# Kernel optimization log

Hardware: AMD Instinct MI355X
Metric: run time of the kernel (lower is better)

The kernel has to match this reference:

```python
import jax, jax.numpy as jnp
import numpy as np

DIM = 1024
DIM_HEAD = 64
HEADS = 16
INNER = DIM_HEAD * HEADS  # 1024
B, N1, N2 = 8, 4096, 256
EPS = 1e-5


def layer_norm(x, w, b):
    mu = jnp.mean(x, axis=-1, keepdims=True)
    var = jnp.var(x, axis=-1, keepdims=True)
    return (x - mu) * jax.lax.rsqrt(var + EPS) * w + b


def setup_inputs() -> dict:
    key = jax.random.key(0)
    ks = jax.random.split(key, 10)
    return {
        "x": jax.random.normal(ks[0], (B, N1, DIM), jnp.float32),
        "latents": jax.random.normal(ks[1], (B, N2, DIM), jnp.float32),
        "shift": jax.random.normal(ks[2], (B, DIM), jnp.float32),
        "scale": jax.random.normal(ks[3], (B, DIM), jnp.float32),
        "ln1_w": jnp.ones((DIM,), jnp.float32),
        "ln1_b": jnp.zeros((DIM,), jnp.float32),
        "ln2_w": jnp.ones((DIM,), jnp.float32),
        "ln2_b": jnp.zeros((DIM,), jnp.float32),
        "Wq": jax.random.normal(ks[4], (INNER, DIM), jnp.float32) * 0.02,
        "Wkv": jax.random.normal(ks[5], (2 * INNER, DIM), jnp.float32) * 0.02,
        "Wo": jax.random.normal(ks[6], (DIM, INNER), jnp.float32) * 0.02,
    }


def reference(x, latents, shift, scale, ln1_w, ln1_b, ln2_w, ln2_b, Wq, Wkv, Wo):
    x = layer_norm(x, ln1_w, ln1_b)                      # (b, n1, D)
    lat = layer_norm(latents, ln2_w, ln2_b)              # (b, n2, D)
    lat = lat * (1.0 + scale[:, None, :]) + shift[:, None, :]

    b, n2, _ = lat.shape
    q = jnp.einsum('bld,ed->ble', lat, Wq)               # (b, n2, inner)
    kv_in = jnp.concatenate((x, lat), axis=-2)           # (b, n1+n2, D)
    kv = jnp.einsum('bld,ed->ble', kv_in, Wkv)           # (b, n1+n2, 2*inner)
    k, v = jnp.split(kv, 2, axis=-1)

    def to_heads(t):
        bsz, L, _ = t.shape
        return t.reshape(bsz, L, HEADS, DIM_HEAD).transpose(0, 2, 1, 3)

    q, k, v = to_heads(q), to_heads(k), to_heads(v)      # (b, h, L, dh)
    attn_scale = 1.0 / np.sqrt(np.sqrt(DIM_HEAD)).astype(np.float32)
    logits = jnp.einsum('bhqd,bhkd->bhqk', q * attn_scale, k * attn_scale)
    w = jax.nn.softmax(logits.astype(jnp.float32), axis=-1).astype(logits.dtype)
    out = jnp.einsum('bhqk,bhkd->bhqd', w, v)            # (b, h, n2, dh)
    out = out.transpose(0, 2, 1, 3).reshape(b, n2, INNER)
    return jnp.einsum('ble,de->bld', out, Wo)            # (b, n2, D)
```

## Files before the change

kernel.cpp:

```cpp
#include <hip/hip_runtime.h>
#include <cstdint>
#include <cstddef>

#define B_SZ 8
#define N1 4096
#define N2 256
#define LTOT 4352
#define DIMD 1024
#define HEADS 16
#define DH 64
#define MKV (B_SZ * LTOT)
#define ATILE 64
#define AITERS (LTOT / ATILE)

typedef _Float16 f16;
typedef f16 f16x4_t __attribute__((ext_vector_type(4)));
typedef f16 f16x8_t __attribute__((ext_vector_type(8)));
typedef float f32x4_t __attribute__((ext_vector_type(4)));

__device__ __forceinline__ void g2l16(const void* g, void* l) {
  __builtin_amdgcn_global_load_lds(
      (__attribute__((address_space(1))) void*)g,
      (__attribute__((address_space(3))) void*)l, 16, 0, 0);
}

__global__ __launch_bounds__(256) void ln_mod_kernel(
    const float* __restrict__ x, const float* __restrict__ lat,
    const float* __restrict__ shift, const float* __restrict__ scale,
    const float* __restrict__ ln1w, const float* __restrict__ ln1b,
    const float* __restrict__ ln2w, const float* __restrict__ ln2b,
    f16* __restrict__ kv_in) {
  const int row = blockIdx.x;
  const int b = row / LTOT;
  const int n = row - b * LTOT;
  const int tid = threadIdx.x;
  const bool is_lat = (n >= N1);
  const float* src = is_lat ? (lat + (size_t)(b * N2 + (n - N1)) * DIMD)
                            : (x + (size_t)(b * N1 + n) * DIMD);
  float4 v = ((const float4*)src)[tid];
  float s = v.x + v.y + v.z + v.w;
  float s2 = v.x * v.x + v.y * v.y + v.z * v.z + v.w * v.w;
#pragma unroll
  for (int m = 1; m <= 32; m <<= 1) {
    s += __shfl_xor(s, m, 64);
    s2 += __shfl_xor(s2, m, 64);
  }
  __shared__ float red[8];
  const int wave = tid >> 6;
  if ((tid & 63) == 0) { red[wave * 2] = s; red[wave * 2 + 1] = s2; }
  __syncthreads();
  s = red[0] + red[2] + red[4] + red[6];
  s2 = red[1] + red[3] + red[5] + red[7];
  const float mean = s * (1.0f / DIMD);
  const float var = fmaxf(s2 * (1.0f / DIMD) - mean * mean, 0.0f);
  const float rstd = rsqrtf(var + 1e-5f);
  const float4 w4 = ((const float4*)(is_lat ? ln2w : ln1w))[tid];
  const float4 b4 = ((const float4*)(is_lat ? ln2b : ln1b))[tid];
  float y0 = (v.x - mean) * rstd * w4.x + b4.x;
  float y1 = (v.y - mean) * rstd * w4.y + b4.y;
  float y2 = (v.z - mean) * rstd * w4.z + b4.z;
  float y3 = (v.w - mean) * rstd * w4.w + b4.w;
  if (is_lat) {
    float4 sc = ((const float4*)(scale + (size_t)b * DIMD))[tid];
    float4 sh = ((const float4*)(shift + (size_t)b * DIMD))[tid];
    y0 = y0 * (1.0f + sc.x) + sh.x;
    y1 = y1 * (1.0f + sc.y) + sh.y;
    y2 = y2 * (1.0f + sc.z) + sh.z;
    y3 = y3 * (1.0f + sc.w) + sh.w;
  }
  f16x4_t o = {(f16)y0, (f16)y1, (f16)y2, (f16)y3};
  *(f16x4_t*)(kv_in + (size_t)row * DIMD + tid * 4) = o;
}

__global__ __launch_bounds__(256) void cast_kernel(const float* __restrict__ in,
                                                   f16* __restrict__ out, int n4) {
  const int i = blockIdx.x * 256 + threadIdx.x;
  if (i < n4) {
    float4 v = ((const float4*)in)[i];
    f16x4_t o = {(f16)v.x, (f16)v.y, (f16)v.z, (f16)v.w};
    ((f16x4_t*)out)[i] = o;
  }
}

template <int MODE>
__global__ __launch_bounds__(256) void gemm128(
    const f16* __restrict__ A0, const f16* __restrict__ BT,
    void* __restrict__ out0, void* __restrict__ out1, int nt_base) {
  const int mt = blockIdx.y, nt = nt_base + blockIdx.x;
  const f16* Abase;
  if (MODE == 1) {
    const int bb = mt >> 1;
    Abase = A0 + ((size_t)(bb * LTOT + N1 + (mt & 1) * 128)) * DIMD;
  } else {
    Abase = A0 + (size_t)mt * 128 * DIMD;
  }
  const f16* Bbase = BT + (size_t)nt * 128 * DIMD;
  __shared__ alignas(16) f16 As[128 * 32];
  __shared__ alignas(16) f16 Bs[128 * 32];
  const int tid = threadIdx.x;
  const int wave = tid >> 6, lane = tid & 63;
  const int wm = (wave & 1) * 64, wn = (wave >> 1) * 64;
  const int lrow = lane >> 2, lcol = (lane & 3) * 8;
  const int r16 = lane & 15, g8 = (lane >> 4) * 8, q4 = (lane >> 4) * 4;
  f32x4_t acc[4][4] = {};
  for (int k0 = 0; k0 < DIMD; k0 += 32) {
    __syncthreads();
    g2l16(Abase + (size_t)(wave * 16 + lrow) * DIMD + k0 + lcol, &As[(wave * 16) * 32]);
    g2l16(Abase + (size_t)(64 + wave * 16 + lrow) * DIMD + k0 + lcol, &As[(64 + wave * 16) * 32]);
    g2l16(Bbase + (size_t)(wave * 16 + lrow) * DIMD + k0 + lcol, &Bs[(wave * 16) * 32]);
    g2l16(Bbase + (size_t)(64 + wave * 16 + lrow) * DIMD + k0 + lcol, &Bs[(64 + wave * 16) * 32]);
    __syncthreads();
    f16x8_t a[4], bf[4];
#pragma unroll
    for (int i = 0; i < 4; i++)
      a[i] = *(const f16x8_t*)&As[(wm + i * 16 + r16) * 32 + g8];
#pragma unroll
    for (int j = 0; j < 4; j++)
      bf[j] = *(const f16x8_t*)&Bs[(wn + j * 16 + r16) * 32 + g8];
#pragma unroll
    for (int i = 0; i < 4; i++)
#pragma unroll
      for (int j = 0; j < 4; j++)
        acc[i][j] = __builtin_amdgcn_mfma_f32_16x16x32_f16(a[i], bf[j], acc[i][j], 0, 0, 0);
  }

  if constexpr (MODE == 0) {
    const int m0 = mt * 128;
    const int b = m0 / LTOT;
    const int n0 = m0 - b * LTOT;
    const int e0 = nt * 128;
    if (e0 < 1024) {
      f16* kbuf = (f16*)out0;
#pragma unroll
      for (int i = 0; i < 4; i++) {
        const int n_base = n0 + wm + i * 16 + q4;
#pragma unroll
        for (int j = 0; j < 4; j++) {
          const int e = e0 + wn + j * 16 + r16;
          const int h = e >> 6, d = e & 63;
          const size_t base = ((size_t)(b * HEADS + h) * LTOT);
#pragma unroll
          for (int r = 0; r < 4; r++)
            kbuf[(base + n_base + r) * DH + d] = (f16)acc[i][j][r];
        }
      }
    } else {
      f16* vbuf = (f16*)out1;
      const int e0v = e0 - 1024;
#pragma unroll
      for (int i = 0; i < 4; i++) {
        const int n_base = n0 + wm + i * 16 + q4;
#pragma unroll
        for (int j = 0; j < 4; j++) {
          const int e = e0v + wn + j * 16 + r16;
          const int h = e >> 6, d = e & 63;
          f16x4_t pk = {(f16)acc[i][j][0], (f16)acc[i][j][1],
                        (f16)acc[i][j][2], (f16)acc[i][j][3]};
          *(f16x4_t*)&vbuf[((size_t)(b * HEADS + h) * DH + d) * LTOT + n_base] = pk;
        }
      }
    }
  } else if constexpr (MODE == 1) {
    f16* qbuf = (f16*)out0;
    const int b = mt >> 1;
#pragma unroll
    for (int i = 0; i < 4; i++) {
      const int n_base = (mt & 1) * 128 + wm + i * 16 + q4;
#pragma unroll
      for (int j = 0; j < 4; j++) {
        const int e = nt * 128 + wn + j * 16 + r16;
        const int h = e >> 6, d = e & 63;
#pragma unroll
        for (int r = 0; r < 4; r++)
          qbuf[((size_t)(b * HEADS + h) * N2 + n_base + r) * DH + d] = (f16)acc[i][j][r];
      }
    }
  } else {
    float* outp = (float*)out0;
    const int m0 = mt * 128;
#pragma unroll
    for (int i = 0; i < 4; i++) {
#pragma unroll
      for (int j = 0; j < 4; j++) {
        const int col = nt * 128 + wn + j * 16 + r16;
#pragma unroll
        for (int r = 0; r < 4; r++)
          outp[(size_t)(m0 + wm + i * 16 + q4 + r) * DIMD + col] = acc[i][j][r];
      }
    }
  }
}

__global__ __launch_bounds__(512, 1) void attn_kernel(
    const f16* __restrict__ qbuf, const f16* __restrict__ kbuf,
    const f16* __restrict__ vbuf, f16* __restrict__ attn_out) {
  const int bh = blockIdx.x >> 1;
  const int qt = blockIdx.x & 1;
  const int b = bh >> 4, h = bh & 15;
  const f16* qg = qbuf + ((size_t)bh * N2 + qt * 128) * DH;
  const f16* kg = kbuf + (size_t)bh * LTOT * DH;
  const f16* vg = vbuf + (size_t)bh * DH * LTOT;

  __shared__ alignas(16) f16 Ks[2][4096];
  __shared__ alignas(16) f16 Vs[2][4096];
  __shared__ alignas(16) f16 QP[9216];

  const int tid = threadIdx.x, wave = tid >> 6, lane = tid & 63;
  const int lrow = lane >> 2, lcol = (lane & 3) * 8;
  const int r16 = lane & 15, g8 = (lane >> 4) * 8, q4 = (lane >> 4) * 4;
  f16* Ps = &QP[wave * 1152];

#pragma unroll
  for (int i = 0; i < 2; i++) {
    const int c = wave * 2 + i, s = c >> 3, rb = (c & 7) * 16;
    g2l16(qg + (size_t)(rb + lrow) * DH + s * 32 + lcol, &QP[s * 4096 + rb * 32]);
  }
  auto stage = [&](int kt, int buf) {
    const int s = wave >> 2, rb = (wave & 3) * 16;
    g2l16(kg + (size_t)(kt * ATILE + rb + lrow) * DH + s * 32 + lcol,
          &Ks[buf][s * 2048 + rb * 32]);
    g2l16(vg + (size_t)(rb + lrow) * LTOT + kt * ATILE + s * 32 + lcol,
          &Vs[buf][s * 2048 + rb * 32]);
  };
  stage(0, 0);
  stage(1, 1);
  asm volatile("s_waitcnt vmcnt(4)" ::: "memory");
  asm volatile("s_barrier" ::: "memory");
  f16x8_t bQ[2];
#pragma unroll
  for (int s = 0; s < 2; s++)
    bQ[s] = *(const f16x8_t*)&QP[s * 4096 + (wave * 16 + r16) * 32 + g8];
  asm volatile("s_waitcnt lgkmcnt(0)" ::: "memory");

  f32x4_t oacc[4] = {};
  float mrow = -1e30f, lsum = 0.0f;
  const float SCL = 0.125f * 1.44269504089f;

  for (int kt = 0; kt < AITERS; kt++) {
    const int cur = kt & 1;
    asm volatile("s_waitcnt vmcnt(2)" ::: "memory");
    asm volatile("s_barrier" ::: "memory");
    f32x4_t sacc[4] = {};
#pragma unroll
    for (int s = 0; s < 2; s++) {
      f16x8_t aK[4];
#pragma unroll
      for (int i = 0; i < 4; i++)
        aK[i] = *(const f16x8_t*)&Ks[cur][s * 2048 + (i * 16 + r16) * 32 + g8];
#pragma unroll
      for (int i = 0; i < 4; i++)
        sacc[i] = __builtin_amdgcn_mfma_f32_16x16x32_f16(aK[i], bQ[s], sacc[i], 0, 0, 0);
    }
    float vmax = -1e30f;
#pragma unroll
    for (int i = 0; i < 4; i++)
#pragma unroll
      for (int r = 0; r < 4; r++) vmax = fmaxf(vmax, sacc[i][r]);
    vmax = fmaxf(vmax, __shfl_xor(vmax, 16, 64));
    vmax = fmaxf(vmax, __shfl_xor(vmax, 32, 64));
    const float m_new = fmaxf(mrow, SCL * vmax);
    const float alpha = exp2f(mrow - m_new);
    float psum = 0.0f;
#pragma unroll
    for (int i = 0; i < 4; i++) {
      f16x4_t pk;
#pragma unroll
      for (int r = 0; r < 4; r++) {
        const float p = exp2f(SCL * sacc[i][r] - m_new);
        psum += p;
        pk[r] = (f16)p;
      }
      *(f16x4_t*)&Ps[r16 * 72 + i * 16 + q4] = pk;
    }
    psum += __shfl_xor(psum, 16, 64);
    psum += __shfl_xor(psum, 32, 64);
    lsum = lsum * alpha + psum;
    mrow = m_new;
#pragma unroll
    for (int id = 0; id < 4; id++) oacc[id] *= alpha;
#pragma unroll
    for (int s2 = 0; s2 < 2; s2++) {
      f16x8_t aV[4];
#pragma unroll
      for (int id = 0; id < 4; id++)
        aV[id] = *(const f16x8_t*)&Vs[cur][s2 * 2048 + (id * 16 + r16) * 32 + g8];
      const f16x8_t bP = *(const f16x8_t*)&Ps[r16 * 72 + s2 * 32 + g8];
#pragma unroll
      for (int id = 0; id < 4; id++)
        oacc[id] = __builtin_amdgcn_mfma_f32_16x16x32_f16(aV[id], bP, oacc[id], 0, 0, 0);
    }
    asm volatile("s_waitcnt lgkmcnt(0)" ::: "memory");
    asm volatile("s_barrier" ::: "memory");
    if (kt + 2 < AITERS) stage(kt + 2, cur);
  }
  const float inv = 1.0f / lsum;
  const int q = qt * 128 + wave * 16 + r16;
  const size_t rowbase = ((size_t)(b * N2 + q)) * DIMD + h * DH;
#pragma unroll
  for (int id = 0; id < 4; id++) {
    f16x4_t pk;
#pragma unroll
    for (int r = 0; r < 4; r++) pk[r] = (f16)(oacc[id][r] * inv);
    *(f16x4_t*)&attn_out[rowbase + id * 16 + q4] = pk;
  }
}

extern "C" void kernel_launch(void* const* d_in, const int* in_sizes, int n_in,
                              void* d_out, int out_size, void* d_ws, size_t ws_size,
                              hipStream_t stream) {
  const float* x     = (const float*)d_in[0];
  const float* lat   = (const float*)d_in[1];
  const float* shift = (const float*)d_in[2];
  const float* scale = (const float*)d_in[3];
  const float* ln1w  = (const float*)d_in[4];
  const float* ln1b  = (const float*)d_in[5];
  const float* ln2w  = (const float*)d_in[6];
  const float* ln2b  = (const float*)d_in[7];
  const float* Wq    = (const float*)d_in[8];
  const float* Wkv   = (const float*)d_in[9];
  const float* Wo    = (const float*)d_in[10];
  float* outp = (float*)d_out;

  char* ws = (char*)d_ws;
  f16* kv_in = (f16*)ws;                 ws += (size_t)MKV * DIMD * 2;
  f16* Wq16  = (f16*)ws;                 ws += (size_t)1024 * 1024 * 2;
  f16* Wkv16 = (f16*)ws;                 ws += (size_t)2048 * 1024 * 2;
  f16* Wo16  = (f16*)ws;                 ws += (size_t)1024 * 1024 * 2;
  f16* qbuf  = (f16*)ws;                 ws += (size_t)B_SZ * HEADS * N2 * DH * 2;
  f16* kbuf  = (f16*)ws;                 ws += (size_t)B_SZ * HEADS * LTOT * DH * 2;
  f16* vbuf  = (f16*)ws;                 ws += (size_t)B_SZ * HEADS * LTOT * DH * 2;
  f16* aout  = (f16*)ws;                 ws += (size_t)B_SZ * N2 * DIMD * 2;

  ln_mod_kernel<<<dim3(MKV), dim3(256), 0, stream>>>(x, lat, shift, scale, ln1w,
                                                     ln1b, ln2w, ln2b, kv_in);
  cast_kernel<<<dim3(1024), dim3(256), 0, stream>>>(Wq, Wq16, 1024 * 1024 / 4);
  cast_kernel<<<dim3(2048), dim3(256), 0, stream>>>(Wkv, Wkv16, 2048 * 1024 / 4);
  cast_kernel<<<dim3(1024), dim3(256), 0, stream>>>(Wo, Wo16, 1024 * 1024 / 4);

  gemm128<0><<<dim3(8, MKV / 128), dim3(256), 0, stream>>>(kv_in, Wkv16, kbuf, vbuf, 0);
  gemm128<0><<<dim3(8, MKV / 128), dim3(256), 0, stream>>>(kv_in, Wkv16, kbuf, vbuf, 8);
  gemm128<1><<<dim3(8, 16), dim3(256), 0, stream>>>(kv_in, Wq16, qbuf, nullptr, 0);
  attn_kernel<<<dim3(256), dim3(512), 0, stream>>>(qbuf, kbuf, vbuf, aout);
  gemm128<2><<<dim3(8, 16), dim3(256), 0, stream>>>(aout, Wo16, outp, nullptr, 0);
}
```

Before: 579.4 us.

## Merge prep and projection launches, remap KV GEMM tiles per XCD

Folds the layernorm kernel and three weight-cast kernels into one prep launch. It also merges the two KV GEMM halves and the Q GEMM into a single launch whose block IDs are remapped so that each XCD works on a contiguous set of M tiles, improving L2 reuse of the A rows. The attention kernel's launch bounds now allow two blocks per CU. This cuts launch count and tail effects, at the cost of possible register pressure in attention from the occupancy hint.

After: 539.8 us. 1.07x faster.

```diff
diff --git a/kernel.cpp b/kernel.cpp
--- a/kernel.cpp
+++ b/kernel.cpp
@@ -12,6 +12,8 @@
 #define MKV (B_SZ * LTOT)
 #define ATILE 64
 #define AITERS (LTOT / ATILE)
+#define G0_BLOCKS 4352
+#define MT_PER_XCD 34
 
 typedef _Float16 f16;
 typedef f16 f16x4_t __attribute__((ext_vector_type(4)));
@@ -24,16 +26,33 @@
       (__attribute__((address_space(3))) void*)l, 16, 0, 0);
 }
 
-__global__ __launch_bounds__(256) void ln_mod_kernel(
+__global__ __launch_bounds__(256) void prep_kernel(
     const float* __restrict__ x, const float* __restrict__ lat,
     const float* __restrict__ shift, const float* __restrict__ scale,
     const float* __restrict__ ln1w, const float* __restrict__ ln1b,
     const float* __restrict__ ln2w, const float* __restrict__ ln2b,
-    f16* __restrict__ kv_in) {
-  const int row = blockIdx.x;
+    const float* __restrict__ Wq, const float* __restrict__ Wkv,
+    const float* __restrict__ Wo, f16* __restrict__ kv_in,
+    f16* __restrict__ Wq16, f16* __restrict__ Wkv16, f16* __restrict__ Wo16) {
+  const int bid = blockIdx.x;
+  const int tid = threadIdx.x;
+  if (bid >= MKV) {
+    const int c = bid - MKV;
+    const float* src;
+    f16* dst;
+    int off;
+    if (c < 1024) { src = Wq; dst = Wq16; off = c; }
+    else if (c < 3072) { src = Wkv; dst = Wkv16; off = c - 1024; }
+    else { src = Wo; dst = Wo16; off = c - 3072; }
+    const int i = off * 256 + tid;
+    float4 v = ((const float4*)src)[i];
+    f16x4_t o = {(f16)v.x, (f16)v.y, (f16)v.z, (f16)v.w};
+    ((f16x4_t*)dst)[i] = o;
+    return;
+  }
+  const int row = bid;
   const int b = row / LTOT;
   const int n = row - b * LTOT;
-  const int tid = threadIdx.x;
   const bool is_lat = (n >= N1);
   const float* src = is_lat ? (lat + (size_t)(b * N2 + (n - N1)) * DIMD)
                             : (x + (size_t)(b * N1 + n) * DIMD);
@@ -72,28 +91,113 @@
   *(f16x4_t*)(kv_in + (size_t)row * DIMD + tid * 4) = o;
 }
 
-__global__ __launch_bounds__(256) void cast_kernel(const float* __restrict__ in,
-                                                   f16* __restrict__ out, int n4) {
-  const int i = blockIdx.x * 256 + threadIdx.x;
-  if (i < n4) {
-    float4 v = ((const float4*)in)[i];
-    f16x4_t o = {(f16)v.x, (f16)v.y, (f16)v.z, (f16)v.w};
-    ((f16x4_t*)out)[i] = o;
-  }
-}
-
-template <int MODE>
-__global__ __launch_bounds__(256) void gemm128(
+__global__ __launch_bounds__(256) void gemm_pre(
+    const f16* __restrict__ kv_in, const f16* __restrict__ Wkv16,
+    const f16* __restrict__ Wq16, f16* __restrict__ kbuf,
+    f16* __restrict__ vbuf, f16* __restrict__ qbuf) {
+  const int id = blockIdx.x;
+  const bool is_kv = (id < G0_BLOCKS);
+  int mt, nt;
+  const f16 *Abase, *Bbase;
+  if (is_kv) {
+    const int xcd = id & 7, l = id >> 3;
+    mt = xcd * MT_PER_XCD + (l >> 4);
+    nt = l & 15;
+    Abase = kv_in + (size_t)mt * 128 * DIMD;
+    Bbase = Wkv16 + (size_t)nt * 128 * DIMD;
+  } else {
+    const int id2 = id - G0_BLOCKS;
+    mt = id2 >> 3;
+    nt = id2 & 7;
+    const int bb = mt >> 1;
+    Abase = kv_in + ((size_t)(bb * LTOT + N1 + (mt & 1) * 128)) * DIMD;
+    Bbase = Wq16 + (size_t)nt * 128 * DIMD;
+  }
+  __shared__ alignas(16) f16 As[128 * 32];
+  __shared__ alignas(16) f16 Bs[128 * 32];
+  const int tid = threadIdx.x;
+  const int wave = tid >> 6, lane = tid & 63;
+  const int wm = (wave & 1) * 64, wn = (wave >> 1) * 64;
+  const int lrow = lane >> 2, lcol = (lane & 3) * 8;
+  const int r16 = lane & 15, g8 = (lane >> 4) * 8, q4 = (lane >> 4) * 4;
+  f32x4_t acc[4][4] = {};
+  for (int k0 = 0; k0 < DIMD; k0 += 32) {
+    __syncthreads();
+    g2l16(Abase + (size_t)(wave * 16 + lrow) * DIMD + k0 + lcol, &As[(wave * 16) * 32]);
+    g2l16(Abase + (size_t)(64 + wave * 16 + lrow) * DIMD + k0 + lcol, &As[(64 + wave * 16) * 32]);
+    g2l16(Bbase + (size_t)(wave * 16 + lrow) * DIMD + k0 + lcol, &Bs[(wave * 16) * 32]);
+    g2l16(Bbase + (size_t)(64 + wave * 16 + lrow) * DIMD + k0 + lcol, &Bs[(64 + wave * 16) * 32]);
+    __syncthreads();
+    f16x8_t a[4], bf[4];
+#pragma unroll
+    for (int i = 0; i < 4; i++)
+      a[i] = *(const f16x8_t*)&As[(wm + i * 16 + r16) * 32 + g8];
+#pragma unroll
+    for (int j = 0; j < 4; j++)
+      bf[j] = *(const f16x8_t*)&Bs[(wn + j * 16 + r16) * 32 + g8];
+#pragma unroll
+    for (int i = 0; i < 4; i++)
+#pragma unroll
+      for (int j = 0; j < 4; j++)
+        acc[i][j] = __builtin_amdgcn_mfma_f32_16x16x32_f16(a[i], bf[j], acc[i][j], 0, 0, 0);
+  }
+
+  if (is_kv) {
+    const int m0 = mt * 128;
+    const int b = m0 / LTOT;
+    const int n0 = m0 - b * LTOT;
+    const int e0 = nt * 128;
+    if (e0 < 1024) {
+#pragma unroll
+      for (int i = 0; i < 4; i++) {
+        const int n_base = n0 + wm + i * 16 + q4;
+#pragma unroll
+        for (int j = 0; j < 4; j++) {
+          const int e = e0 + wn + j * 16 + r16;
+          const int h = e >> 6, d = e & 63;
+          const size_t base = ((size_t)(b * HEADS + h) * LTOT);
+#pragma unroll
+          for (int r = 0; r < 4; r++)
+            kbuf[(base + n_base + r) * DH + d] = (f16)acc[i][j][r];
+        }
+      }
+    } else {
+      const int e0v = e0 - 1024;
+#pragma unroll
+      for (int i = 0; i < 4; i++) {
+        const int n_base = n0 + wm + i * 16 + q4;
+#pragma unroll
+        for (int j = 0; j < 4; j++) {
+          const int e = e0v + wn + j * 16 + r16;
+          const int h = e >> 6, d = e & 63;
+          f16x4_t pk = {(f16)acc[i][j][0], (f16)acc[i][j][1],
+                        (f16)acc[i][j][2], (f16)acc[i][j][3]};
+          *(f16x4_t*)&vbuf[((size_t)(b * HEADS + h) * DH + d) * LTOT + n_base] = pk;
+        }
+      }
+    }
+  } else {
+    const int b = mt >> 1;
+#pragma unroll
+    for (int i = 0; i < 4; i++) {
+      const int n_base = (mt & 1) * 128 + wm + i * 16 + q4;
+#pragma unroll
+      for (int j = 0; j < 4; j++) {
+        const int e = nt * 128 + wn + j * 16 + r16;
+        const int h = e >> 6, d = e & 63;
+#pragma unroll
+        for (int r = 0; r < 4; r++)
+          qbuf[((size_t)(b * HEADS + h) * N2 + n_base + r) * DH + d] = (f16)acc[i][j][r];
+      }
+    }
+  }
+}
+
+__global__ __launch_bounds__(256) void gemm_out(
     const f16* __restrict__ A0, const f16* __restrict__ BT,
-    void* __restrict__ out0, void* __restrict__ out1, int nt_base) {
-  const int mt = blockIdx.y, nt = nt_base + blockIdx.x;
-  const f16* Abase;
-  if (MODE == 1) {
-    const int bb = mt >> 1;
-    Abase = A0 + ((size_t)(bb * LTOT + N1 + (mt & 1) * 128)) * DIMD;
-  } else {
-    Abase = A0 + (size_t)mt * 128 * DIMD;
-  }
+    float* __restrict__ outp) {
+  const int mt = blockIdx.y, nt = blockIdx.x;
+  const f16* Abase = A0 + (size_t)mt * 128 * DIMD;
   const f16* Bbase = BT + (size_t)nt * 128 * DIMD;
   __shared__ alignas(16) f16 As[128 * 32];
   __shared__ alignas(16) f16 Bs[128 * 32];
@@ -123,75 +227,20 @@
       for (int j = 0; j < 4; j++)
         acc[i][j] = __builtin_amdgcn_mfma_f32_16x16x32_f16(a[i], bf[j], acc[i][j], 0, 0, 0);
   }
-
-  if constexpr (MODE == 0) {
-    const int m0 = mt * 128;
-    const int b = m0 / LTOT;
-    const int n0 = m0 - b * LTOT;
-    const int e0 = nt * 128;
-    if (e0 < 1024) {
-      f16* kbuf = (f16*)out0;
-#pragma unroll
-      for (int i = 0; i < 4; i++) {
-        const int n_base = n0 + wm + i * 16 + q4;
-#pragma unroll
-        for (int j = 0; j < 4; j++) {
-          const int e = e0 + wn + j * 16 + r16;
-          const int h = e >> 6, d = e & 63;
-          const size_t base = ((size_t)(b * HEADS + h) * LTOT);
-#pragma unroll
-          for (int r = 0; r < 4; r++)
-            kbuf[(base + n_base + r) * DH + d] = (f16)acc[i][j][r];
-        }
-      }
-    } else {
-      f16* vbuf = (f16*)out1;
-      const int e0v = e0 - 1024;
-#pragma unroll
-      for (int i = 0; i < 4; i++) {
-        const int n_base = n0 + wm + i * 16 + q4;
-#pragma unroll
-        for (int j = 0; j < 4; j++) {
-          const int e = e0v + wn + j * 16 + r16;
-          const int h = e >> 6, d = e & 63;
-          f16x4_t pk = {(f16)acc[i][j][0], (f16)acc[i][j][1],
-                        (f16)acc[i][j][2], (f16)acc[i][j][3]};
-          *(f16x4_t*)&vbuf[((size_t)(b * HEADS + h) * DH + d) * LTOT + n_base] = pk;
-        }
-      }
-    }
-  } else if constexpr (MODE == 1) {
-    f16* qbuf = (f16*)out0;
-    const int b = mt >> 1;
-#pragma unroll
-    for (int i = 0; i < 4; i++) {
-      const int n_base = (mt & 1) * 128 + wm + i * 16 + q4;
-#pragma unroll
-      for (int j = 0; j < 4; j++) {
-        const int e = nt * 128 + wn + j * 16 + r16;
-        const int h = e >> 6, d = e & 63;
-#pragma unroll
-        for (int r = 0; r < 4; r++)
-          qbuf[((size_t)(b * HEADS + h) * N2 + n_base + r) * DH + d] = (f16)acc[i][j][r];
-      }
-    }
-  } else {
-    float* outp = (float*)out0;
-    const int m0 = mt * 128;
-#pragma unroll
-    for (int i = 0; i < 4; i++) {
-#pragma unroll
-      for (int j = 0; j < 4; j++) {
-        const int col = nt * 128 + wn + j * 16 + r16;
-#pragma unroll
-        for (int r = 0; r < 4; r++)
-          outp[(size_t)(m0 + wm + i * 16 + q4 + r) * DIMD + col] = acc[i][j][r];
-      }
-    }
-  }
-}
-
-__global__ __launch_bounds__(512, 1) void attn_kernel(
+  const int m0 = mt * 128;
+#pragma unroll
+  for (int i = 0; i < 4; i++) {
+#pragma unroll
+    for (int j = 0; j < 4; j++) {
+      const int col = nt * 128 + wn + j * 16 + r16;
+#pragma unroll
+      for (int r = 0; r < 4; r++)
+        outp[(size_t)(m0 + wm + i * 16 + q4 + r) * DIMD + col] = acc[i][j][r];
+    }
+  }
+}
+
+__global__ __launch_bounds__(512, 2) void attn_kernel(
     const f16* __restrict__ qbuf, const f16* __restrict__ kbuf,
     const f16* __restrict__ vbuf, f16* __restrict__ attn_out) {
   const int bh = blockIdx.x >> 1;
@@ -331,15 +380,11 @@
   f16* vbuf  = (f16*)ws;                 ws += (size_t)B_SZ * HEADS * LTOT * DH * 2;
   f16* aout  = (f16*)ws;                 ws += (size_t)B_SZ * N2 * DIMD * 2;
 
-  ln_mod_kernel<<<dim3(MKV), dim3(256), 0, stream>>>(x, lat, shift, scale, ln1w,
-                                                     ln1b, ln2w, ln2b, kv_in);
-  cast_kernel<<<dim3(1024), dim3(256), 0, stream>>>(Wq, Wq16, 1024 * 1024 / 4);
-  cast_kernel<<<dim3(2048), dim3(256), 0, stream>>>(Wkv, Wkv16, 2048 * 1024 / 4);
-  cast_kernel<<<dim3(1024), dim3(256), 0, stream>>>(Wo, Wo16, 1024 * 1024 / 4);
-
-  gemm128<0><<<dim3(8, MKV / 128), dim3(256), 0, stream>>>(kv_in, Wkv16, kbuf, vbuf, 0);
-  gemm128<0><<<dim3(8, MKV / 128), dim3(256), 0, stream>>>(kv_in, Wkv16, kbuf, vbuf, 8);
-  gemm128<1><<<dim3(8, 16), dim3(256), 0, stream>>>(kv_in, Wq16, qbuf, nullptr, 0);
+  prep_kernel<<<dim3(MKV + 4096), dim3(256), 0, stream>>>(
+      x, lat, shift, scale, ln1w, ln1b, ln2w, ln2b, Wq, Wkv, Wo,
+      kv_in, Wq16, Wkv16, Wo16);
+  gemm_pre<<<dim3(G0_BLOCKS + 128), dim3(256), 0, stream>>>(
+      kv_in, Wkv16, Wq16, kbuf, vbuf, qbuf);
   attn_kernel<<<dim3(256), dim3(512), 0, stream>>>(qbuf, kbuf, vbuf, aout);
-  gemm128<2><<<dim3(8, 16), dim3(256), 0, stream>>>(aout, Wo16, outp, nullptr, 0);
-}
+  gemm_out<<<dim3(8, 16), dim3(256), 0, stream>>>(aout, Wo16, outp);
+}
```
